# Optimization experiments

Hardware: AMD Instinct MI355X
Metric: run time of the kernel (lower is better)

## Reference

```python
import jax, jax.numpy as jnp
import numpy as np

THETA = 20.0
DIRECTIONS = [[i, j, k] for i in (-1, 0, 1) for j in (-1, 0, 1) for k in (-1, 0, 1)
              if (i, j, k) != (0, 0, 0)]  # 26 neighbor directions, torch-loop order


def _shift(x, d):
    """Zero-padded shift along spatial axes (1,2,3) by direction d in {-1,0,1}^3.
    d[i]==+1: out[..., :-1, ...] = x[..., 1:, ...] (edge slice -> 0), matching the
    torch slice-assignment in the original forward."""
    for ax, s in zip((1, 2, 3), d):
        if s == 0:
            continue
        pad = [(0, 0)] * x.ndim
        if s == 1:
            pad[ax] = (0, 1)
            x = jax.lax.slice_in_dim(jnp.pad(x, pad), 1, x.shape[ax] + 1, axis=ax)
        else:
            pad[ax] = (1, 0)
            x = jax.lax.slice_in_dim(jnp.pad(x, pad), 0, x.shape[ax], axis=ax)
    return x


def _kld(inp, tgt):
    # torch.nn.KLDivLoss(reduction='none'): xlogy(t, t) - t * inp (0 where t == 0)
    safe = jnp.where(tgt > 0, tgt, 1.0)
    return jnp.where(tgt > 0, tgt * jnp.log(safe), 0.0) - tgt * inp


def _dt1d(f, axis):
    # exact 1D squared distance transform: out[i] = min_j f[j] + (i - j)^2
    L = f.shape[axis]
    fm = jnp.moveaxis(f, axis, -1)  # [..., L]
    idx = jnp.arange(L, dtype=f.dtype)
    def step(carry, i):
        return carry, jnp.min(fm + (i - idx) ** 2, axis=-1)
    _, out = jax.lax.scan(step, None, idx)  # [L, ...]
    return jnp.moveaxis(jnp.moveaxis(out, 0, -1), -1, axis)


def _edt(boundary):
    # per-batch exact Euclidean distance to nearest True voxel (== scipy
    # distance_transform_edt((gdb==0)) with sampling [inf,1,1,1])
    BIG = 1e10
    f = jnp.where(boundary, 0.0, BIG)
    for ax in (1, 2, 3):
        f = _dt1d(f, ax)
    return jnp.sqrt(f)


def _forward(inp, target):
    theta = THETA
    preds = jnp.transpose(inp, (0, 2, 3, 4, 1))  # [B,D,H,W,C]
    B, D, H, W, C = preds.shape

    # --- predicted boundary detection: neighbor KL along W, H, D ---
    kl_h = jnp.mean(_kld(preds, _shift(preds, (0, 0, 1))), axis=-1)
    kl_h = kl_h.at[:, :, :, -1].set(-1.0)
    kl_v = jnp.mean(_kld(preds, _shift(preds, (0, 1, 0))), axis=-1)
    kl_v = kl_v.at[:, :, -1, :].set(-1.0)
    kl_d = jnp.mean(_kld(preds, _shift(preds, (1, 0, 0))), axis=-1)
    kl_d = kl_d.at[:, -1, :, :].set(-1.0)
    kl_vals = jnp.maximum(jnp.maximum(kl_h, kl_v), kl_d)  # [B,D,H,W]
    thr = jnp.quantile(kl_vals, 0.99)
    pdb_mask = kl_vals >= thr  # dense stand-in for torch.nonzero gather

    # --- ground-truth boundary + distance transform ---
    gt_h = _shift(target, (0, 0, 1))
    gt_v = _shift(target, (0, 1, 0))
    gt_d = _shift(target, (1, 0, 0))
    gdb = (target * 3) != (gt_h + gt_v + gt_d)  # [B,D,H,W] bool
    gdb_dist = jax.lax.stop_gradient(_edt(gdb))

    # coordinate grids: original (buggy but faithful) code masks using index
    # columns 0,1,2 of the nonzero tensor, i.e. (batch, d, h) coordinates
    coord = [jnp.arange(B)[:, None, None, None],
             jnp.arange(D)[None, :, None, None],
             jnp.arange(H)[None, None, :, None]]
    spatial = (D, H, W)

    d_pi_cols, dist_cols = [], []
    for d in DIRECTIONS:
        sh = jax.lax.stop_gradient(_shift(preds, d))  # .detach() in original
        kl = jnp.exp(jnp.mean(_kld(preds, sh), axis=-1))  # [B,D,H,W]
        for i in range(3):
            if d[i] == 1:
                z = spatial[i] - 1
            elif d[i] == -1:
                z = 0
            else:
                z = 1
            if z != 1:
                kl = jnp.where(coord[i] == z, kl, 0.0)
        d_pi_cols.append(kl)
        dist_cols.append(_shift(gdb_dist, d))  # zero-padded shift, like dist_array
    d_pi = jnp.stack(d_pi_cols, axis=-1)    # [B,D,H,W,26]
    dists = jnp.stack(dist_cols, axis=-1)   # [B,D,H,W,26]

    s = jnp.sum(d_pi, axis=-1, keepdims=True)
    d_pi = d_pi / jnp.where(s == 0, 1.0, s)  # sum>0 at every pdb pixel when B==1

    min_idx = jnp.argmin(dists, axis=-1)  # first min, like torch.argmin
    d_gi = jnp.where(jnp.arange(len(DIRECTIONS)) == min_idx[..., None],
                     0.8, 0.2 / len(DIRECTIONS))

    # BCEWithLogitsLoss(reduction='none')
    x, y = d_pi, d_gi
    bce = jnp.maximum(x, 0.0) - x * y + jnp.log1p(jnp.exp(-jnp.abs(x)))

    weight = jnp.minimum(gdb_dist, theta) / theta
    loss = weight * jnp.mean(bce, axis=-1)
    loss = jnp.where(gdb_dist != 0, loss, 0.0)

    n_pdb = jnp.sum(pdb_mask).astype(preds.dtype)
    total = jnp.sum(jnp.where(pdb_mask, loss, 0.0)) / n_pdb
    return total


def setup_inputs() -> dict:
    key = jax.random.key(0)
    k1, k2 = jax.random.split(key)
    inp = jax.random.uniform(k1, (1, 2, 48, 160, 160), dtype=jnp.float32)
    target = jax.random.randint(k2, (1, 48, 160, 160), 0, 2, dtype=jnp.int32)
    return {"inp": inp, "target": target}


def reference(inp, target):
    return _forward(inp, target)
```

## Files before the change

kernel.cpp:

```cpp
#include <hip/hip_runtime.h>
#include <math.h>

#define D_ 48
#define H_ 160
#define W_ 160
#define HW_ 25600
#define N_ 1228800
#define NBLK 4800
#define HBLK 600
#define K1_ 1216512u

static_assert(N_ == D_ * HW_, "dims");
static_assert(N_ == NBLK * 256, "grid");
static_assert(N_ == HBLK * 256 * 8, "hist grid");

#define OFF_KL   0u
#define OFF_FA   (N_ * 4u)
#define OFF_FB   (2u * N_ * 4u)
#define OFF_CAND (3u * N_ * 4u)
#define OFF_G1   (4u * N_ * 4u)
#define OFF_SC   (OFF_G1 + 4096u * 4u)
#define OFF_PS   (OFF_SC + 64u)
#define OFF_PC   (OFF_PS + NBLK * 4u)

__device__ __forceinline__ unsigned fkey(float v) {
  unsigned u = __float_as_uint(v);
  return (u & 0x80000000u) ? ~u : (u | 0x80000000u);
}

__global__ __launch_bounds__(256) void k_zero(unsigned* __restrict__ g1,
                                              unsigned* __restrict__ sc) {
  const int i = blockIdx.x * 256 + threadIdx.x;
  if (i < 4096) g1[i] = 0u;
  else if (i < 4112) sc[i - 4096] = 0u;
}

__global__ __launch_bounds__(256) void k_prep(const float* __restrict__ inp,
                                              const int* __restrict__ tgt,
                                              float* __restrict__ kl,
                                              float* __restrict__ f0,
                                              unsigned* __restrict__ ghist) {
  __shared__ unsigned h[4096];
  const int tid = threadIdx.x;
  for (int i = tid; i < 4096; i += 256) h[i] = 0;
  __syncthreads();
  const int base = blockIdx.x * 2048;
  for (int e = 0; e < 8; e++) {
    const int idx = base + e * 256 + tid;
    const int ww = idx % W_;
    const int hh = (idx / W_) % H_;
    const int dd = idx / HW_;
    const float p0 = inp[idx];
    const float p1 = inp[N_ + idx];

    float klh = -1.0f, klv = -1.0f, kld = -1.0f;
    if (ww < W_ - 1) {
      const float t0 = inp[idx + 1], t1 = inp[N_ + idx + 1];
      const float a0 = (t0 > 0.f) ? t0 * logf(t0) : 0.f;
      const float a1 = (t1 > 0.f) ? t1 * logf(t1) : 0.f;
      klh = 0.5f * ((a0 - t0 * p0) + (a1 - t1 * p1));
    }
    if (hh < H_ - 1) {
      const float t0 = inp[idx + W_], t1 = inp[N_ + idx + W_];
      const float a0 = (t0 > 0.f) ? t0 * logf(t0) : 0.f;
      const float a1 = (t1 > 0.f) ? t1 * logf(t1) : 0.f;
      klv = 0.5f * ((a0 - t0 * p0) + (a1 - t1 * p1));
    }
    if (dd < D_ - 1) {
      const float t0 = inp[idx + HW_], t1 = inp[N_ + idx + HW_];
      const float a0 = (t0 > 0.f) ? t0 * logf(t0) : 0.f;
      const float a1 = (t1 > 0.f) ? t1 * logf(t1) : 0.f;
      kld = 0.5f * ((a0 - t0 * p0) + (a1 - t1 * p1));
    }
    const float kmax = fmaxf(fmaxf(klh, klv), kld);
    kl[idx] = kmax;
    atomicAdd(&h[fkey(kmax) >> 20], 1u);

    const int tv = tgt[idx];
    const int t1 = (ww < W_ - 1) ? tgt[idx + 1] : 0;
    const int t2 = (hh < H_ - 1) ? tgt[idx + W_] : 0;
    const int t3 = (dd < D_ - 1) ? tgt[idx + HW_] : 0;
    f0[idx] = (3 * tv != t1 + t2 + t3) ? 0.f : 1e10f;
  }
  __syncthreads();
  for (int i = tid; i < 4096; i += 256) {
    const unsigned c = h[i];
    if (c) atomicAdd(&ghist[i], c);
  }
}

__global__ __launch_bounds__(256) void k_dt_d(const float* __restrict__ fin,
                                              float* __restrict__ fout,
                                              const unsigned* __restrict__ g1,
                                              unsigned* __restrict__ sc) {
  const int idx = blockIdx.x * 256 + threadIdx.x;
  const int pos = idx / HW_;
  float m = fin[idx];
  for (int r = 1; r < D_; r++) {
    const float r2 = (float)(r * r);
    if (r2 >= m) break;
    const bool okm = (pos - r >= 0), okp = (pos + r < D_);
    if (!okm && !okp) break;
    if (okm) m = fminf(m, fin[idx - r * HW_] + r2);
    if (okp) m = fminf(m, fin[idx + r * HW_] + r2);
  }
  fout[idx] = m;

  if (blockIdx.x == 0) {
    __shared__ unsigned ssum[256];
    const int t = threadIdx.x;
    unsigned s = 0;
#pragma unroll
    for (int i = 0; i < 16; i++) s += g1[t * 16 + i];
    const unsigned mine = s;
    ssum[t] = s;
    __syncthreads();
    for (int o = 1; o < 256; o <<= 1) {
      const unsigned add = (t >= o) ? ssum[t - o] : 0u;
      __syncthreads();
      ssum[t] += add;
      __syncthreads();
    }
    const unsigned before = ssum[t] - mine;
    if (before < K1_ && K1_ <= before + mine) {
      unsigned cum = before;
      for (int i = 0; i < 16; i++) {
        const unsigned c = g1[t * 16 + i];
        if (cum < K1_ && K1_ <= cum + c) { sc[0] = (unsigned)(t * 16 + i); sc[1] = K1_ - cum; break; }
        cum += c;
      }
    }
  }
}

__global__ __launch_bounds__(256) void k_dt_h(const float* __restrict__ fin,
                                              float* __restrict__ fout,
                                              const float* __restrict__ kl,
                                              unsigned* __restrict__ cand,
                                              unsigned* __restrict__ sc) {
  const int tid = threadIdx.x;
  const int base = blockIdx.x * 2048;
  const unsigned b1 = sc[0];
  unsigned keys[8];
  unsigned kmask = 0u;
#pragma unroll
  for (int e = 0; e < 8; e++) {
    const int idx = base + e * 256 + tid;
    const int pos = (idx / W_) % H_;
    float m = fin[idx];
    for (int r = 1; r < H_; r++) {
      const float r2 = (float)(r * r);
      if (r2 >= m) break;
      const bool okm = (pos - r >= 0), okp = (pos + r < H_);
      if (!okm && !okp) break;
      if (okm) m = fminf(m, fin[idx - r * W_] + r2);
      if (okp) m = fminf(m, fin[idx + r * W_] + r2);
    }
    fout[idx] = m;
    const unsigned key = fkey(kl[idx]);
    keys[e] = key & 0xFFFFFu;
    if ((key >> 20) == b1) kmask |= (1u << e);
  }
  const unsigned cnt = (unsigned)__popc(kmask);
  __shared__ unsigned scnt[256];
  __shared__ unsigned sbase;
  scnt[tid] = cnt;
  __syncthreads();
  for (int o = 1; o < 256; o <<= 1) {
    const unsigned add = (tid >= o) ? scnt[tid - o] : 0u;
    __syncthreads();
    scnt[tid] += add;
    __syncthreads();
  }
  if (tid == 255 && scnt[255] > 0) sbase = atomicAdd(&sc[8], scnt[255]);
  __syncthreads();
  if (cnt) {
    const unsigned wb = sbase + scnt[tid] - cnt;
#pragma unroll
    for (int e = 0; e < 8; e++) {
      if (kmask & (1u << e)) cand[wb + __popc(kmask & ((1u << e) - 1u))] = keys[e];
    }
  }
}

__global__ __launch_bounds__(256) void k_dt_w(const float* __restrict__ fin,
                                              float* __restrict__ fout,
                                              const unsigned* __restrict__ cand,
                                              unsigned* __restrict__ sc) {
  const int idx = blockIdx.x * 256 + threadIdx.x;
  const int pos = idx % W_;
  float m = fin[idx];
  for (int r = 1; r < W_; r++) {
    const float r2 = (float)(r * r);
    if (r2 >= m) break;
    const bool okm = (pos - r >= 0), okp = (pos + r < W_);
    if (!okm && !okp) break;
    if (okm) m = fminf(m, fin[idx - r] + r2);
    if (okp) m = fminf(m, fin[idx + r] + r2);
  }
  fout[idx] = sqrtf(m);

  if (blockIdx.x != 0) return;
  const int tid = threadIdx.x;
  const unsigned M = sc[8];
  const unsigned K = sc[1];
  __shared__ unsigned hist[4096];
  __shared__ unsigned ssum[256];
  __shared__ unsigned sBA, sKB;
  for (int i = tid; i < 4096; i += 256) hist[i] = 0;
  __syncthreads();
  const unsigned M4 = M & ~3u;
  for (unsigned g = (unsigned)tid; g * 4u < M4; g += 256u) {
    const uint4 v = *reinterpret_cast<const uint4*>(&cand[g * 4u]);
    atomicAdd(&hist[(v.x >> 8) & 0xFFFu], 1u);
    atomicAdd(&hist[(v.y >> 8) & 0xFFFu], 1u);
    atomicAdd(&hist[(v.z >> 8) & 0xFFFu], 1u);
    atomicAdd(&hist[(v.w >> 8) & 0xFFFu], 1u);
  }
  for (unsigned i = M4 + (unsigned)tid; i < M; i += 256u) atomicAdd(&hist[(cand[i] >> 8) & 0xFFFu], 1u);
  __syncthreads();
  unsigned mine = 0;
#pragma unroll
  for (int i = 0; i < 16; i++) mine += hist[tid * 16 + i];
  ssum[tid] = mine;
  __syncthreads();
  for (int o = 1; o < 256; o <<= 1) {
    const unsigned add = (tid >= o) ? ssum[tid - o] : 0u;
    __syncthreads();
    ssum[tid] += add;
    __syncthreads();
  }
  {
    const unsigned before = ssum[tid] - mine;
    if (before < K && K <= before + mine) {
      unsigned cum = before;
      for (int i = 0; i < 16; i++) {
        const unsigned c = hist[tid * 16 + i];
        if (cum < K && K <= cum + c) { sBA = (unsigned)(tid * 16 + i); sKB = K - cum; break; }
        cum += c;
      }
    }
  }
  __syncthreads();
  const unsigned bA = sBA, KB = sKB;
  __shared__ unsigned h2[256];
  h2[tid] = 0;
  __syncthreads();
  for (unsigned g = (unsigned)tid; g * 4u < M4; g += 256u) {
    const uint4 v = *reinterpret_cast<const uint4*>(&cand[g * 4u]);
    if (((v.x >> 8) & 0xFFFu) == bA) atomicAdd(&h2[v.x & 0xFFu], 1u);
    if (((v.y >> 8) & 0xFFFu) == bA) atomicAdd(&h2[v.y & 0xFFu], 1u);
    if (((v.z >> 8) & 0xFFFu) == bA) atomicAdd(&h2[v.z & 0xFFu], 1u);
    if (((v.w >> 8) & 0xFFFu) == bA) atomicAdd(&h2[v.w & 0xFFu], 1u);
  }
  for (unsigned i = M4 + (unsigned)tid; i < M; i += 256u) {
    const unsigned v = cand[i];
    if (((v >> 8) & 0xFFFu) == bA) atomicAdd(&h2[v & 0xFFu], 1u);
  }
  __syncthreads();
  const unsigned mine2 = h2[tid];
  ssum[tid] = mine2;
  __syncthreads();
  for (int o = 1; o < 256; o <<= 1) {
    const unsigned add = (tid >= o) ? ssum[tid - o] : 0u;
    __syncthreads();
    ssum[tid] += add;
    __syncthreads();
  }
  {
    const unsigned before = ssum[tid] - mine2;
    if (before < KB && KB <= before + mine2) {
      const unsigned key = (sc[0] << 20) | (bA << 8) | (unsigned)tid;
      sc[6] = (key & 0x80000000u) ? (key & 0x7FFFFFFFu) : ~key;
    }
  }
}

__global__ __launch_bounds__(256) void k_loss(const float* __restrict__ inp,
                                              const float* __restrict__ kl,
                                              const float* __restrict__ gdist,
                                              const unsigned* __restrict__ sc,
                                              float* __restrict__ psum,
                                              unsigned* __restrict__ pcnt) {
  const int tid = threadIdx.x;
  const int idx = blockIdx.x * 256 + tid;
  const float thr = __uint_as_float(sc[6]);
  float myloss = 0.f;
  unsigned mycnt = 0u;
  if (kl[idx] >= thr) {
    mycnt = 1u;
    const float g = gdist[idx];
    if (g != 0.f) {
      const int ww = idx % W_;
      const int hh = (idx / W_) % H_;
      const int dd = idx / HW_;
      const float p0 = inp[idx];
      const float p1 = inp[N_ + idx];
      constexpr int DI[26] = {-1,-1,-1,-1,-1,-1,-1,-1,-1, 0,0,0,0,0,0,0,0, 1,1,1,1,1,1,1,1,1};
      constexpr int DJ[26] = {-1,-1,-1, 0,0,0, 1,1,1, -1,-1,-1, 0,0, 1,1,1, -1,-1,-1, 0,0,0, 1,1,1};
      constexpr int DK[26] = {-1,0,1, -1,0,1, -1,0,1, -1,0,1, -1,1, -1,0,1, -1,0,1, -1,0,1, -1,0,1};
      float klv[26], dst[26];
      float s = 0.f;
#pragma unroll
      for (int t = 0; t < 26; t++) {
        const int nd = dd + DI[t], nh = hh + DJ[t], nw = ww + DK[t];
        const bool inb = ((unsigned)nd < (unsigned)D_) && ((unsigned)nh < (unsigned)H_) &&
                         ((unsigned)nw < (unsigned)W_);
        const int nidx = (nd * H_ + nh) * W_ + nw;
        dst[t] = inb ? gdist[nidx] : 0.f;
        bool keep;
        if (DI[t] == 1 || DJ[t] == 1) keep = false;
        else {
          keep = true;
          if (DJ[t] == -1) keep = (dd == 0);
          if (DK[t] == 1) keep = keep && (hh == H_ - 1);
          if (DK[t] == -1) keep = keep && (hh == 0);
        }
        float kt = 0.f;
        if (keep) {
          float t0 = 0.f, t1 = 0.f;
          if (inb) { t0 = inp[nidx]; t1 = inp[N_ + nidx]; }
          const float a0 = (t0 > 0.f) ? t0 * logf(t0) : 0.f;
          const float a1 = (t1 > 0.f) ? t1 * logf(t1) : 0.f;
          const float kldm = 0.5f * ((a0 - t0 * p0) + (a1 - t1 * p1));
          kt = expf(kldm);
        }
        klv[t] = kt;
        s += kt;
      }
      const float denom = (s == 0.f) ? 1.f : s;
      int amin = 0;
      float dmin = dst[0];
#pragma unroll
      for (int t = 1; t < 26; t++) {
        if (dst[t] < dmin) { dmin = dst[t]; amin = t; }
      }
      const float yoff = (float)(0.2 / 26.0);
      float bsum = 0.f;
#pragma unroll
      for (int t = 0; t < 26; t++) {
        const float x = klv[t] / denom;
        const float y = (t == amin) ? 0.8f : yoff;
        bsum += fmaxf(x, 0.f) - x * y + log1pf(expf(-fabsf(x)));
      }
      myloss = (fminf(g, 20.f) / 20.f) * (bsum / 26.f);
    }
  }
  __shared__ float ls[256];
  __shared__ unsigned lc[256];
  ls[tid] = myloss;
  lc[tid] = mycnt;
  __syncthreads();
  for (int o = 128; o > 0; o >>= 1) {
    if (tid < o) { ls[tid] += ls[tid + o]; lc[tid] += lc[tid + o]; }
    __syncthreads();
  }
  if (tid == 0) { psum[blockIdx.x] = ls[0]; pcnt[blockIdx.x] = lc[0]; }
}

__global__ __launch_bounds__(256) void k_reduce(const float* __restrict__ psum,
                                                const unsigned* __restrict__ pcnt,
                                                float* __restrict__ out) {
  __shared__ float ls[256];
  __shared__ unsigned lc[256];
  const int t = threadIdx.x;
  float s = 0.f;
  unsigned c = 0;
  for (int g = t; g * 4 < NBLK; g += 256) {
    const float4 s4 = *reinterpret_cast<const float4*>(&psum[g * 4]);
    const uint4 c4 = *reinterpret_cast<const uint4*>(&pcnt[g * 4]);
    s += (s4.x + s4.y) + (s4.z + s4.w);
    c += c4.x + c4.y + c4.z + c4.w;
  }
  ls[t] = s;
  lc[t] = c;
  __syncthreads();
  for (int o = 128; o > 0; o >>= 1) {
    if (t < o) { ls[t] += ls[t + o]; lc[t] += lc[t + o]; }
    __syncthreads();
  }
  if (t == 0) out[0] = ls[0] / (float)lc[0];
}

extern "C" void kernel_launch(void* const* d_in, const int* in_sizes, int n_in,
                              void* d_out, int out_size, void* d_ws, size_t ws_size,
                              hipStream_t stream) {
  (void)in_sizes; (void)n_in; (void)out_size; (void)ws_size;
  const float* inp = (const float*)d_in[0];
  const int* tgt = (const int*)d_in[1];
  float* out = (float*)d_out;
  char* ws = (char*)d_ws;

  float* kl = (float*)(ws + OFF_KL);
  float* fA = (float*)(ws + OFF_FA);
  float* fB = (float*)(ws + OFF_FB);
  unsigned* cand = (unsigned*)(ws + OFF_CAND);
  unsigned* g1 = (unsigned*)(ws + OFF_G1);
  unsigned* sc = (unsigned*)(ws + OFF_SC);
  float* ps = (float*)(ws + OFF_PS);
  unsigned* pc = (unsigned*)(ws + OFF_PC);

  k_zero<<<17, 256, 0, stream>>>(g1, sc);
  k_prep<<<HBLK, 256, 0, stream>>>(inp, tgt, kl, fA, g1);
  k_dt_d<<<NBLK, 256, 0, stream>>>(fA, fB, g1, sc);
  k_dt_h<<<HBLK, 256, 0, stream>>>(fB, fA, kl, cand, sc);
  k_dt_w<<<NBLK, 256, 0, stream>>>(fA, fB, cand, sc);
  k_loss<<<NBLK, 256, 0, stream>>>(inp, kl, fB, sc, ps, pc);
  k_reduce<<<1, 256, 0, stream>>>(ps, pc, out);
}
```

Baseline: 86.41 us.

## Replace global atomic candidate compaction with per-block slots and wave ballot

```diff
diff --git a/kernel.cpp b/kernel.cpp
--- a/kernel.cpp
+++ b/kernel.cpp
@@ -22,6 +22,7 @@
 #define OFF_SC   (OFF_G1 + 4096u * 4u)
 #define OFF_PS   (OFF_SC + 64u)
 #define OFF_PC   (OFF_PS + NBLK * 4u)
+#define OFF_CNT  (OFF_PC + NBLK * 4u)
 
 __device__ __forceinline__ unsigned fkey(float v) {
   unsigned u = __float_as_uint(v);
@@ -137,55 +138,42 @@
                                               float* __restrict__ fout,
                                               const float* __restrict__ kl,
                                               unsigned* __restrict__ cand,
-                                              unsigned* __restrict__ sc) {
+                                              unsigned* __restrict__ cnt,
+                                              const unsigned* __restrict__ sc) {
   const int tid = threadIdx.x;
-  const int base = blockIdx.x * 2048;
-  const unsigned b1 = sc[0];
-  unsigned keys[8];
-  unsigned kmask = 0u;
-#pragma unroll
-  for (int e = 0; e < 8; e++) {
-    const int idx = base + e * 256 + tid;
-    const int pos = (idx / W_) % H_;
-    float m = fin[idx];
-    for (int r = 1; r < H_; r++) {
-      const float r2 = (float)(r * r);
-      if (r2 >= m) break;
-      const bool okm = (pos - r >= 0), okp = (pos + r < H_);
-      if (!okm && !okp) break;
-      if (okm) m = fminf(m, fin[idx - r * W_] + r2);
-      if (okp) m = fminf(m, fin[idx + r * W_] + r2);
-    }
-    fout[idx] = m;
-    const unsigned key = fkey(kl[idx]);
-    keys[e] = key & 0xFFFFFu;
-    if ((key >> 20) == b1) kmask |= (1u << e);
-  }
-  const unsigned cnt = (unsigned)__popc(kmask);
-  __shared__ unsigned scnt[256];
-  __shared__ unsigned sbase;
-  scnt[tid] = cnt;
-  __syncthreads();
-  for (int o = 1; o < 256; o <<= 1) {
-    const unsigned add = (tid >= o) ? scnt[tid - o] : 0u;
-    __syncthreads();
-    scnt[tid] += add;
-    __syncthreads();
-  }
-  if (tid == 255 && scnt[255] > 0) sbase = atomicAdd(&sc[8], scnt[255]);
-  __syncthreads();
-  if (cnt) {
-    const unsigned wb = sbase + scnt[tid] - cnt;
-#pragma unroll
-    for (int e = 0; e < 8; e++) {
-      if (kmask & (1u << e)) cand[wb + __popc(kmask & ((1u << e) - 1u))] = keys[e];
-    }
-  }
+  const int idx = blockIdx.x * 256 + tid;
+  const int pos = (idx / W_) % H_;
+  float m = fin[idx];
+  for (int r = 1; r < H_; r++) {
+    const float r2 = (float)(r * r);
+    if (r2 >= m) break;
+    const bool okm = (pos - r >= 0), okp = (pos + r < H_);
+    if (!okm && !okp) break;
+    if (okm) m = fminf(m, fin[idx - r * W_] + r2);
+    if (okp) m = fminf(m, fin[idx + r * W_] + r2);
+  }
+  fout[idx] = m;
+
+  const unsigned key = fkey(kl[idx]);
+  const bool has = ((key >> 20) == sc[0]);
+  const unsigned long long bal = __ballot(has);
+  const int lane = tid & 63;
+  const int wid = tid >> 6;
+  const unsigned lpre = (unsigned)__popcll(bal & ((1ULL << lane) - 1ULL));
+  const unsigned wtot = (unsigned)__popcll(bal);
+  __shared__ unsigned wcnt[4];
+  if (lane == 0) wcnt[wid] = wtot;
+  __syncthreads();
+  unsigned off = 0;
+  for (int w = 0; w < wid; w++) off += wcnt[w];
+  if (has) cand[blockIdx.x * 256 + off + lpre] = key & 0xFFFFFu;
+  if (tid == 0) cnt[blockIdx.x] = wcnt[0] + wcnt[1] + wcnt[2] + wcnt[3];
 }
 
 __global__ __launch_bounds__(256) void k_dt_w(const float* __restrict__ fin,
                                               float* __restrict__ fout,
                                               const unsigned* __restrict__ cand,
+                                              const unsigned* __restrict__ cnt,
                                               unsigned* __restrict__ sc) {
   const int idx = blockIdx.x * 256 + threadIdx.x;
   const int pos = idx % W_;
@@ -202,22 +190,19 @@
 
   if (blockIdx.x != 0) return;
   const int tid = threadIdx.x;
-  const unsigned M = sc[8];
   const unsigned K = sc[1];
   __shared__ unsigned hist[4096];
   __shared__ unsigned ssum[256];
+  __shared__ unsigned h2[256];
   __shared__ unsigned sBA, sKB;
   for (int i = tid; i < 4096; i += 256) hist[i] = 0;
-  __syncthreads();
-  const unsigned M4 = M & ~3u;
-  for (unsigned g = (unsigned)tid; g * 4u < M4; g += 256u) {
-    const uint4 v = *reinterpret_cast<const uint4*>(&cand[g * 4u]);
-    atomicAdd(&hist[(v.x >> 8) & 0xFFFu], 1u);
-    atomicAdd(&hist[(v.y >> 8) & 0xFFFu], 1u);
-    atomicAdd(&hist[(v.z >> 8) & 0xFFFu], 1u);
-    atomicAdd(&hist[(v.w >> 8) & 0xFFFu], 1u);
-  }
-  for (unsigned i = M4 + (unsigned)tid; i < M; i += 256u) atomicAdd(&hist[(cand[i] >> 8) & 0xFFFu], 1u);
+  h2[tid] = 0;
+  __syncthreads();
+  for (int b = tid; b < NBLK; b += 256) {
+    const unsigned c = cnt[b];
+    const unsigned rb = (unsigned)b * 256u;
+    for (unsigned i = 0; i < c; i++) atomicAdd(&hist[(cand[rb + i] >> 8) & 0xFFFu], 1u);
+  }
   __syncthreads();
   unsigned mine = 0;
 #pragma unroll
@@ -243,19 +228,13 @@
   }
   __syncthreads();
   const unsigned bA = sBA, KB = sKB;
-  __shared__ unsigned h2[256];
-  h2[tid] = 0;
-  __syncthreads();
-  for (unsigned g = (unsigned)tid; g * 4u < M4; g += 256u) {
-    const uint4 v = *reinterpret_cast<const uint4*>(&cand[g * 4u]);
-    if (((v.x >> 8) & 0xFFFu) == bA) atomicAdd(&h2[v.x & 0xFFu], 1u);
-    if (((v.y >> 8) & 0xFFFu) == bA) atomicAdd(&h2[v.y & 0xFFu], 1u);
-    if (((v.z >> 8) & 0xFFFu) == bA) atomicAdd(&h2[v.z & 0xFFu], 1u);
-    if (((v.w >> 8) & 0xFFFu) == bA) atomicAdd(&h2[v.w & 0xFFu], 1u);
-  }
-  for (unsigned i = M4 + (unsigned)tid; i < M; i += 256u) {
-    const unsigned v = cand[i];
-    if (((v >> 8) & 0xFFFu) == bA) atomicAdd(&h2[v & 0xFFu], 1u);
+  for (int b = tid; b < NBLK; b += 256) {
+    const unsigned c = cnt[b];
+    const unsigned rb = (unsigned)b * 256u;
+    for (unsigned i = 0; i < c; i++) {
+      const unsigned v = cand[rb + i];
+      if (((v >> 8) & 0xFFFu) == bA) atomicAdd(&h2[v & 0xFFu], 1u);
+    }
   }
   __syncthreads();
   const unsigned mine2 = h2[tid];
@@ -399,12 +378,13 @@
   unsigned* sc = (unsigned*)(ws + OFF_SC);
   float* ps = (float*)(ws + OFF_PS);
   unsigned* pc = (unsigned*)(ws + OFF_PC);
+  unsigned* cnt = (unsigned*)(ws + OFF_CNT);
 
   k_zero<<<17, 256, 0, stream>>>(g1, sc);
   k_prep<<<HBLK, 256, 0, stream>>>(inp, tgt, kl, fA, g1);
   k_dt_d<<<NBLK, 256, 0, stream>>>(fA, fB, g1, sc);
-  k_dt_h<<<HBLK, 256, 0, stream>>>(fB, fA, kl, cand, sc);
-  k_dt_w<<<NBLK, 256, 0, stream>>>(fA, fB, cand, sc);
+  k_dt_h<<<NBLK, 256, 0, stream>>>(fB, fA, kl, cand, cnt, sc);
+  k_dt_w<<<NBLK, 256, 0, stream>>>(fA, fB, cand, cnt, sc);
   k_loss<<<NBLK, 256, 0, stream>>>(inp, kl, fB, sc, ps, pc);
   k_reduce<<<1, 256, 0, stream>>>(ps, pc, out);
 }
```

New measurement: 106.3 us. +23.0%, slower.
